# Kernel tuning notes

Hardware: AMD Instinct MI355X
Metric: run time of the kernel (lower is better)

Reference implementation:

```python
import jax, jax.numpy as jnp
import numpy as np

# Static multi-level feature-map shapes (H, W) per level.
SPATIAL_SHAPES = np.array([[92, 160], [46, 80], [23, 40], [12, 20]], dtype=np.int32)
NUM_HEADS = 8
NUM_LEVELS = 4
NUM_POINTS = 4      # sampling points per head per level (num_all_points)
NUM_Z = 4           # num_Z_anchors; NUM_POINTS % NUM_Z == 0
EMBED = 256
HEAD_DIM = EMBED // NUM_HEADS


def setup_inputs() -> dict:
    key = jax.random.key(0)
    ks = jax.random.split(key, 10)
    bs, nq = 2, 10000
    nv = int((SPATIAL_SHAPES[:, 0] * SPATIAL_SHAPES[:, 1]).sum())  # 19560
    query = jax.random.normal(ks[0], (bs, nq, EMBED), jnp.float32)
    value = jax.random.normal(ks[1], (bs, nv, EMBED), jnp.float32)
    query_pos = jax.random.normal(ks[2], (bs, nq, EMBED), jnp.float32)
    reference_points = jax.random.uniform(ks[3], (bs, nq, NUM_Z, 2), jnp.float32)
    W_val = jax.random.normal(ks[4], (EMBED, EMBED), jnp.float32) / jnp.sqrt(EMBED)
    b_val = jnp.zeros((EMBED,), jnp.float32)
    W_off = jax.random.normal(ks[5], (EMBED, NUM_HEADS * NUM_LEVELS * NUM_POINTS * 2), jnp.float32) * 0.01
    b_off = jax.random.normal(ks[6], (NUM_HEADS * NUM_LEVELS * NUM_POINTS * 2,), jnp.float32) * 0.5
    W_attn = jax.random.normal(ks[7], (EMBED, NUM_HEADS * NUM_LEVELS * NUM_POINTS), jnp.float32) * 0.02
    b_attn = jnp.zeros((NUM_HEADS * NUM_LEVELS * NUM_POINTS,), jnp.float32)
    spatial_shapes = jnp.asarray(SPATIAL_SHAPES)
    return {
        'query': query, 'value': value, 'query_pos': query_pos,
        'reference_points': reference_points,
        'W_val': W_val, 'b_val': b_val, 'W_off': W_off, 'b_off': b_off,
        'W_attn': W_attn, 'b_attn': b_attn, 'spatial_shapes': spatial_shapes,
    }


def _bilinear(v, x, y, H, W):
    """grid_sample(mode='bilinear', padding_mode='zeros', align_corners=False).

    v: (bs, H, W, heads, d); x, y: (bs, nq, heads, P) pixel coords.
    Returns (bs, nq, heads, P, d).
    """
    x0 = jnp.floor(x)
    y0 = jnp.floor(y)
    wx1 = x - x0
    wy1 = y - y0
    wx0 = 1.0 - wx1
    wy0 = 1.0 - wy1
    x0i = x0.astype(jnp.int32)
    y0i = y0.astype(jnp.int32)
    b = jnp.arange(v.shape[0])[:, None, None, None]
    h = jnp.arange(v.shape[3])[None, None, :, None]

    def gather(yi, xi):
        valid = (yi >= 0) & (yi < H) & (xi >= 0) & (xi < W)
        yc = jnp.clip(yi, 0, H - 1)
        xc = jnp.clip(xi, 0, W - 1)
        g = v[b, yc, xc, h]  # (bs, nq, heads, P, d)
        return g * valid[..., None].astype(v.dtype)

    return (gather(y0i, x0i) * (wy0 * wx0)[..., None]
            + gather(y0i, x0i + 1) * (wy0 * wx1)[..., None]
            + gather(y0i + 1, x0i) * (wy1 * wx0)[..., None]
            + gather(y0i + 1, x0i + 1) * (wy1 * wx1)[..., None])


def reference(query, value, query_pos, reference_points, W_val, b_val,
              W_off, b_off, W_attn, b_attn, spatial_shapes):
    bs, nq, _ = query.shape
    q = query + query_pos
    # value projection -> per-head values
    v = (value @ W_val + b_val).reshape(bs, -1, NUM_HEADS, HEAD_DIM)
    # sampling offsets and attention weights from query
    off = (q @ W_off + b_off).reshape(bs, nq, NUM_HEADS, NUM_LEVELS, NUM_POINTS, 2)
    attn = (q @ W_attn + b_attn).reshape(bs, nq, NUM_HEADS, NUM_LEVELS * NUM_POINTS)
    attn = jax.nn.softmax(attn, axis=-1).reshape(bs, nq, NUM_HEADS, NUM_LEVELS, NUM_POINTS)
    # normalize offsets by (w, h) of each level
    norm = jnp.stack([spatial_shapes[:, 1], spatial_shapes[:, 0]], -1).astype(q.dtype)  # (L, 2)
    off = off / norm[None, None, None, :, None, :]
    # fold Z-anchor reference points in, matching the shape[-1]==2 branch
    off = off.reshape(bs, nq, NUM_HEADS, NUM_LEVELS, NUM_POINTS // NUM_Z, NUM_Z, 2)
    loc = reference_points[:, :, None, None, None, :, :] + off
    loc = loc.reshape(bs, nq, NUM_HEADS, NUM_LEVELS, NUM_POINTS, 2)
    grid = 2.0 * loc - 1.0  # grid_sample convention

    start = 0
    sampled = []
    for lvl in range(NUM_LEVELS):
        H, W = int(SPATIAL_SHAPES[lvl, 0]), int(SPATIAL_SHAPES[lvl, 1])
        vl = v[:, start:start + H * W].reshape(bs, H, W, NUM_HEADS, HEAD_DIM)
        start += H * W
        # align_corners=False pixel coords
        x = ((grid[:, :, :, lvl, :, 0] + 1.0) * W - 1.0) * 0.5
        y = ((grid[:, :, :, lvl, :, 1] + 1.0) * H - 1.0) * 0.5
        sampled.append(_bilinear(vl, x, y, H, W))
    samp = jnp.stack(sampled, axis=3)  # (bs, nq, heads, L, P, d)
    out = (samp * attn[..., None]).sum(axis=(3, 4))  # (bs, nq, heads, d)
    return out.reshape(bs, nq, NUM_HEADS * HEAD_DIM)
```

## Files before the change

kernel.cpp:

```cpp
#include <hip/hip_runtime.h>

#define NQ 10000
#define BS 2
#define NV 19560
#define NH 8
#define HD 32
#define EMB 256

typedef __attribute__((ext_vector_type(8))) short bf16x8;
typedef __attribute__((ext_vector_type(4))) float f32x4;
typedef __attribute__((ext_vector_type(4))) short s16x4;

__device__ __forceinline__ unsigned short f2bf(float x) {
    unsigned u = __float_as_uint(x);
    u += 0x7FFFu + ((u >> 16) & 1u);
    return (unsigned short)(u >> 16);
}

__global__ __launch_bounds__(256) void convert_W(
    const float* __restrict__ Wv, const float* __restrict__ Wo,
    const float* __restrict__ Wa, const float* __restrict__ bv,
    const float* __restrict__ bo, const float* __restrict__ ba,
    ushort* __restrict__ Bt, float* __restrict__ bias) {
    int n = blockIdx.x;
    int k = threadIdx.x;
    float x;
    if (n < 256)       x = Wv[k * 256 + n];
    else if (n < 512)  x = Wo[k * 256 + (n - 256)];
    else               x = Wa[k * 128 + (n - 512)];
    Bt[n * 256 + k] = f2bf(x);
    if (k == 0)
        bias[n] = (n < 256) ? bv[n] : (n < 512) ? bo[n - 256] : ba[n - 512];
}

__global__ __launch_bounds__(256) void gemm_fused(
    const float* __restrict__ value, const float* __restrict__ query,
    const float* __restrict__ qpos, const ushort* __restrict__ Bt,
    const float* __restrict__ bias,
    ushort* __restrict__ Cv, float* __restrict__ C0, float* __restrict__ C1)
{
    __shared__ short As[64][40], Bhs[128][40];

    const int tid = threadIdx.x;
    const int bid = blockIdx.x;
    bool isval; int mblk, npan;
    if (bid < 1224) { isval = true;  mblk = bid >> 1; npan = bid & 1; }
    else { int q = bid - 1224; isval = false; mblk = q / 3; npan = q % 3; }

    const int M  = isval ? (BS * NV) : (BS * NQ);
    const int m0 = mblk * 64;
    const int n0 = npan * 128;
    const int nbase = (isval ? 0 : 256) + n0;

    const float* A = isval ? value : query;

    const int arow = tid >> 2;
    const int acol = (tid & 3) * 8;
    const bool aval = (m0 + arow) < M;
    const float* Ap  = A    + (size_t)(m0 + arow) * 256 + acol;
    const float* A2p = qpos + (size_t)(m0 + arow) * 256 + acol;
    const int brow = tid >> 1;
    const int bcol = (tid & 1) * 16;
    const ushort* Bp = Bt + (size_t)(nbase + brow) * 256 + bcol;

    const int lane = tid & 63, wave = tid >> 6;
    const int wrow = (wave >> 1) * 32, wcol = (wave & 1) * 64;
    const int lr = lane & 15, quad = lane >> 4, lk = quad * 8;

    f32x4 acc[2][4] = {};

    for (int k0 = 0; k0 < 256; k0 += 32) {
        #pragma unroll
        for (int g = 0; g < 2; g++) {
            f32x4 v = {};
            if (aval) {
                v = *(const f32x4*)(Ap + k0 + g * 4);
                if (!isval) v += *(const f32x4*)(A2p + k0 + g * 4);
            }
            s16x4 hh;
            #pragma unroll
            for (int e = 0; e < 4; e++) hh[e] = (short)f2bf(v[e]);
            *(s16x4*)&As[arow][acol + g * 4] = hh;
        }
        *(bf16x8*)&Bhs[brow][bcol]     = *(const bf16x8*)(Bp + k0);
        *(bf16x8*)&Bhs[brow][bcol + 8] = *(const bf16x8*)(Bp + k0 + 8);
        __syncthreads();

        bf16x8 af[2], bhf[4];
        #pragma unroll
        for (int i = 0; i < 2; i++)
            af[i] = *(const bf16x8*)&As[wrow + i * 16 + lr][lk];
        #pragma unroll
        for (int j = 0; j < 4; j++)
            bhf[j] = *(const bf16x8*)&Bhs[wcol + j * 16 + lr][lk];
        #pragma unroll
        for (int i = 0; i < 2; i++)
            #pragma unroll
            for (int j = 0; j < 4; j++)
                acc[i][j] = __builtin_amdgcn_mfma_f32_16x16x32_bf16(af[i], bhf[j], acc[i][j], 0, 0, 0);
        __syncthreads();
    }

    #pragma unroll
    for (int j = 0; j < 4; j++) {
        int cc = wcol + j * 16 + lr;
        int col = n0 + cc;
        float bb = bias[nbase + cc];
        #pragma unroll
        for (int i = 0; i < 2; i++) {
            int gmb = m0 + wrow + i * 16 + quad * 4;
            #pragma unroll
            for (int r = 0; r < 4; r++) {
                int gm = gmb + r;
                if (gm < M) {
                    float val = acc[i][j][r] + bb;
                    if (isval) {
                        int h = col >> 5, d = col & 31;
                        int b = (gm >= NV) ? 1 : 0;
                        int pix = gm - b * NV;
                        Cv[((size_t)(b * 8 + h) * NV + pix) * 32 + d] = f2bf(val);
                    } else {
                        if (col < 256) C0[(size_t)gm * 256 + col] = val;
                        else           C1[(size_t)gm * 128 + (col - 256)] = val;
                    }
                }
            }
        }
    }
}

__global__ __launch_bounds__(256) void sample4(
    const ushort* __restrict__ v, const float* __restrict__ off,
    const float* __restrict__ attn, const float* __restrict__ refp,
    float* __restrict__ out)
{
    __shared__ int   s_off[256][5];
    __shared__ float s_w[256][5];

    const int bq0 = blockIdx.x * 2;
    const int t = threadIdx.x;

    {
        const int bq = bq0 + (t >> 7);
        const int b = (bq >= NQ) ? 1 : 0;
        const int i = t & 127;
        const int h = i >> 4, l = (i >> 2) & 3, p = i & 3;

        float logit = attn[(size_t)bq * 128 + i];
        float mx = logit;
        #pragma unroll
        for (int m = 1; m < 16; m <<= 1) mx = fmaxf(mx, __shfl_xor(mx, m, 16));
        float e = __expf(logit - mx);
        float s = e;
        #pragma unroll
        for (int m = 1; m < 16; m <<= 1) s += __shfl_xor(s, m, 16);
        float w = e / s;

        const float Wf[4] = {160.f, 80.f, 40.f, 20.f};
        const float Hf[4] = {92.f, 46.f, 23.f, 12.f};
        const int   Wi[4] = {160, 80, 40, 20};
        const int   Hi[4] = {92, 46, 23, 12};
        const int   st[4] = {0, 14720, 18400, 19320};

        float ox = off[(size_t)bq * 256 + h * 32 + l * 8 + p * 2];
        float oy = off[(size_t)bq * 256 + h * 32 + l * 8 + p * 2 + 1];
        float rx = refp[(size_t)bq * 8 + p * 2];
        float ry = refp[(size_t)bq * 8 + p * 2 + 1];
        float x = rx * Wf[l] + ox - 0.5f;
        float y = ry * Hf[l] + oy - 0.5f;
        float x0f = floorf(x), y0f = floorf(y);
        float wx1 = x - x0f, wy1 = y - y0f;
        float wx0 = 1.f - wx1, wy0 = 1.f - wy1;
        int x0 = (int)x0f, y0 = (int)y0f;
        const int W = Wi[l], H = Hi[l];
        float mx0 = ((unsigned)x0       < (unsigned)W) ? 1.f : 0.f;
        float mx1 = ((unsigned)(x0 + 1) < (unsigned)W) ? 1.f : 0.f;
        float my0 = ((unsigned)y0       < (unsigned)H) ? 1.f : 0.f;
        float my1 = ((unsigned)(y0 + 1) < (unsigned)H) ? 1.f : 0.f;
        int xc0 = min(max(x0, 0), W - 1);
        int xc1 = min(max(x0 + 1, 0), W - 1);
        int yc0 = min(max(y0, 0), H - 1);
        int yc1 = min(max(y0 + 1, 0), H - 1);
        int base = ((b * 8 + h) * NV + st[l]) * 32;
        s_off[t][0] = base + (yc0 * W + xc0) * 32;
        s_off[t][1] = base + (yc0 * W + xc1) * 32;
        s_off[t][2] = base + (yc1 * W + xc0) * 32;
        s_off[t][3] = base + (yc1 * W + xc1) * 32;
        s_w[t][0] = w * wy0 * wx0 * my0 * mx0;
        s_w[t][1] = w * wy0 * wx1 * my0 * mx1;
        s_w[t][2] = w * wy1 * wx0 * my1 * mx0;
        s_w[t][3] = w * wy1 * wx1 * my1 * mx1;
    }
    __syncthreads();

    const int g = t >> 4;
    const int lane = t & 15;
    const int qi = g >> 3, h = g & 7;
    const int bq = bq0 + qi;
    const int d2 = lane * 2;
    const int pbase = qi * 128 + h * 16;

    float acc0 = 0.f, acc1 = 0.f, acc2 = 0.f, acc3 = 0.f;
    #pragma unroll
    for (int ib = 0; ib < 4; ib++) {
        int o[16]; float wgt[16];
        #pragma unroll
        for (int pp = 0; pp < 4; pp++) {
            int idx = pbase + ib * 4 + pp;
            #pragma unroll
            for (int c = 0; c < 4; c++) {
                o[pp * 4 + c]   = s_off[idx][c];
                wgt[pp * 4 + c] = s_w[idx][c];
            }
        }
        unsigned u[16];
        #pragma unroll
        for (int j = 0; j < 16; j++)
            u[j] = *(const unsigned*)(v + o[j] + d2);
        #pragma unroll
        for (int j = 0; j < 16; j += 2) {
            acc0 += wgt[j]     * __uint_as_float(u[j] << 16);
            acc1 += wgt[j]     * __uint_as_float(u[j] & 0xffff0000u);
            acc2 += wgt[j + 1] * __uint_as_float(u[j + 1] << 16);
            acc3 += wgt[j + 1] * __uint_as_float(u[j + 1] & 0xffff0000u);
        }
    }
    float2 res = make_float2(acc0 + acc2, acc1 + acc3);
    *(float2*)(out + (size_t)bq * 256 + h * 32 + d2) = res;
}

extern "C" void kernel_launch(void* const* d_in, const int* in_sizes, int n_in,
                              void* d_out, int out_size, void* d_ws, size_t ws_size,
                              hipStream_t stream) {
    const float* query     = (const float*)d_in[0];
    const float* value     = (const float*)d_in[1];
    const float* query_pos = (const float*)d_in[2];
    const float* refp      = (const float*)d_in[3];
    const float* W_val     = (const float*)d_in[4];
    const float* b_val     = (const float*)d_in[5];
    const float* W_off     = (const float*)d_in[6];
    const float* b_off     = (const float*)d_in[7];
    const float* W_attn    = (const float*)d_in[8];
    const float* b_attn    = (const float*)d_in[9];
    float* out = (float*)d_out;

    char* w = (char*)d_ws;
    float*  off    = (float*)w;   w += 20480000;
    float*  attn   = (float*)w;   w += 10240000;
    ushort* vp_bf  = (ushort*)w;  w += 20029440;
    ushort* Bt     = (ushort*)w;  w += 327680;
    float*  bias_c = (float*)w;   w += 2560;

    convert_W<<<640, 256, 0, stream>>>(W_val, W_off, W_attn, b_val, b_off, b_attn,
                                       Bt, bias_c);

    gemm_fused<<<1224 + 939, 256, 0, stream>>>(value, query, query_pos, Bt, bias_c,
                                               vp_bf, off, attn);

    sample4<<<BS * NQ / 2, 256, 0, stream>>>(vp_bf, off, attn, refp, out);
}
```

Measured before the change: 220.2 us.

## Load GEMM fragments directly from global memory, dropping LDS staging and barriers

The fused projection GEMM no longer stages A and B tiles through shared memory. Each wave loads its MFMA operand fragments straight from global memory and converts A to bf16 in registers, and the k-loop is fully unrolled. This removes LDS writes and reads and both __syncthreads per k-step. The cost is redundant global loads, since A rows are re-read by the two column waves and B rows by the two row waves, and the loads are narrower and less coalesced. Out-of-range rows are clamped to the last valid row rather than zeroed, and the epilogue still masks them.

```diff
diff --git a/kernel.cpp b/kernel.cpp
--- a/kernel.cpp
+++ b/kernel.cpp
@@ -39,8 +39,6 @@
     const float* __restrict__ bias,
     ushort* __restrict__ Cv, float* __restrict__ C0, float* __restrict__ C1)
 {
-    __shared__ short As[64][40], Bhs[128][40];
-
     const int tid = threadIdx.x;
     const int bid = blockIdx.x;
     bool isval; int mblk, npan;
@@ -54,51 +52,55 @@
 
     const float* A = isval ? value : query;
 
-    const int arow = tid >> 2;
-    const int acol = (tid & 3) * 8;
-    const bool aval = (m0 + arow) < M;
-    const float* Ap  = A    + (size_t)(m0 + arow) * 256 + acol;
-    const float* A2p = qpos + (size_t)(m0 + arow) * 256 + acol;
-    const int brow = tid >> 1;
-    const int bcol = (tid & 1) * 16;
-    const ushort* Bp = Bt + (size_t)(nbase + brow) * 256 + bcol;
-
     const int lane = tid & 63, wave = tid >> 6;
     const int wrow = (wave >> 1) * 32, wcol = (wave & 1) * 64;
     const int lr = lane & 15, quad = lane >> 4, lk = quad * 8;
 
+    const float* Ap[2]; const float* Qp[2];
+    #pragma unroll
+    for (int i = 0; i < 2; i++) {
+        int row = m0 + wrow + i * 16 + lr;
+        if (row >= M) row = M - 1;
+        Ap[i] = A    + (size_t)row * 256 + lk;
+        Qp[i] = qpos + (size_t)row * 256 + lk;
+    }
+    const ushort* Bp[4];
+    #pragma unroll
+    for (int j = 0; j < 4; j++)
+        Bp[j] = Bt + (size_t)(nbase + wcol + j * 16 + lr) * 256 + lk;
+
     f32x4 acc[2][4] = {};
 
+    #pragma unroll
     for (int k0 = 0; k0 < 256; k0 += 32) {
-        #pragma unroll
-        for (int g = 0; g < 2; g++) {
-            f32x4 v = {};
-            if (aval) {
-                v = *(const f32x4*)(Ap + k0 + g * 4);
-                if (!isval) v += *(const f32x4*)(A2p + k0 + g * 4);
-            }
-            s16x4 hh;
-            #pragma unroll
-            for (int e = 0; e < 4; e++) hh[e] = (short)f2bf(v[e]);
-            *(s16x4*)&As[arow][acol + g * 4] = hh;
-        }
-        *(bf16x8*)&Bhs[brow][bcol]     = *(const bf16x8*)(Bp + k0);
-        *(bf16x8*)&Bhs[brow][bcol + 8] = *(const bf16x8*)(Bp + k0 + 8);
-        __syncthreads();
-
-        bf16x8 af[2], bhf[4];
-        #pragma unroll
-        for (int i = 0; i < 2; i++)
-            af[i] = *(const bf16x8*)&As[wrow + i * 16 + lr][lk];
+        bf16x8 bhf[4];
         #pragma unroll
         for (int j = 0; j < 4; j++)
-            bhf[j] = *(const bf16x8*)&Bhs[wcol + j * 16 + lr][lk];
+            bhf[j] = *(const bf16x8*)(Bp[j] + k0);
+
+        bf16x8 af[2];
+        #pragma unroll
+        for (int i = 0; i < 2; i++) {
+            f32x4 lo = *(const f32x4*)(Ap[i] + k0);
+            f32x4 hi = *(const f32x4*)(Ap[i] + k0 + 4);
+            if (!isval) {
+                lo += *(const f32x4*)(Qp[i] + k0);
+                hi += *(const f32x4*)(Qp[i] + k0 + 4);
+            }
+            bf16x8 t;
+            #pragma unroll
+            for (int e = 0; e < 4; e++) {
+                t[e]     = (short)f2bf(lo[e]);
+                t[e + 4] = (short)f2bf(hi[e]);
+            }
+            af[i] = t;
+        }
+
         #pragma unroll
         for (int i = 0; i < 2; i++)
             #pragma unroll
             for (int j = 0; j < 4; j++)
                 acc[i][j] = __builtin_amdgcn_mfma_f32_16x16x32_bf16(af[i], bhf[j], acc[i][j], 0, 0, 0);
-        __syncthreads();
     }
 
     #pragma unroll
```

New measurement: 269.6 us. 22.4% more time.

## Double-buffer GEMM LDS tiles with register prefetch of next K slice

Applied to the files above, without the earlier changes.

The fused projection GEMM now keeps two LDS buffers for the A and B tiles. While MFMAs run on the current K slice, it loads the next slice from global memory into registers, then converts it to bf16 and stores it into the other buffer. This hides global-load latency behind compute and drops one of the two barriers per K step. In exchange it doubles the LDS footprint and raises register pressure, which could lower occupancy.

```diff
diff --git a/kernel.cpp b/kernel.cpp
--- a/kernel.cpp
+++ b/kernel.cpp
@@ -39,7 +39,8 @@
     const float* __restrict__ bias,
     ushort* __restrict__ Cv, float* __restrict__ C0, float* __restrict__ C1)
 {
-    __shared__ short As[64][40], Bhs[128][40];
+    __shared__ __align__(16) short As[2][64][40];
+    __shared__ __align__(16) short Bhs[2][128][40];
 
     const int tid = threadIdx.x;
     const int bid = blockIdx.x;
@@ -69,36 +70,73 @@
 
     f32x4 acc[2][4] = {};
 
-    for (int k0 = 0; k0 < 256; k0 += 32) {
+    {
         #pragma unroll
         for (int g = 0; g < 2; g++) {
             f32x4 v = {};
             if (aval) {
-                v = *(const f32x4*)(Ap + k0 + g * 4);
-                if (!isval) v += *(const f32x4*)(A2p + k0 + g * 4);
+                v = *(const f32x4*)(Ap + g * 4);
+                if (!isval) v += *(const f32x4*)(A2p + g * 4);
             }
             s16x4 hh;
             #pragma unroll
             for (int e = 0; e < 4; e++) hh[e] = (short)f2bf(v[e]);
-            *(s16x4*)&As[arow][acol + g * 4] = hh;
-        }
-        *(bf16x8*)&Bhs[brow][bcol]     = *(const bf16x8*)(Bp + k0);
-        *(bf16x8*)&Bhs[brow][bcol + 8] = *(const bf16x8*)(Bp + k0 + 8);
-        __syncthreads();
+            *(s16x4*)&As[0][arow][acol + g * 4] = hh;
+        }
+        *(bf16x8*)&Bhs[0][brow][bcol]     = *(const bf16x8*)(Bp);
+        *(bf16x8*)&Bhs[0][brow][bcol + 8] = *(const bf16x8*)(Bp + 8);
+    }
+    asm volatile("s_waitcnt lgkmcnt(0)" ::: "memory");
+    __builtin_amdgcn_s_barrier();
+
+    #pragma unroll
+    for (int s = 0; s < 8; s++) {
+        const int cur = s & 1, nxt = cur ^ 1;
+        const int k1 = (s + 1) * 32;
+
+        f32x4 pa0 = {}, pa1 = {}, qa0 = {}, qa1 = {};
+        bf16x8 pb0, pb1;
+        if (s < 7) {
+            if (aval) {
+                pa0 = *(const f32x4*)(Ap + k1);
+                pa1 = *(const f32x4*)(Ap + k1 + 4);
+                if (!isval) {
+                    qa0 = *(const f32x4*)(A2p + k1);
+                    qa1 = *(const f32x4*)(A2p + k1 + 4);
+                }
+            }
+            pb0 = *(const bf16x8*)(Bp + k1);
+            pb1 = *(const bf16x8*)(Bp + k1 + 8);
+        }
 
         bf16x8 af[2], bhf[4];
         #pragma unroll
         for (int i = 0; i < 2; i++)
-            af[i] = *(const bf16x8*)&As[wrow + i * 16 + lr][lk];
+            af[i] = *(const bf16x8*)&As[cur][wrow + i * 16 + lr][lk];
         #pragma unroll
         for (int j = 0; j < 4; j++)
-            bhf[j] = *(const bf16x8*)&Bhs[wcol + j * 16 + lr][lk];
+            bhf[j] = *(const bf16x8*)&Bhs[cur][wcol + j * 16 + lr][lk];
         #pragma unroll
         for (int i = 0; i < 2; i++)
             #pragma unroll
             for (int j = 0; j < 4; j++)
                 acc[i][j] = __builtin_amdgcn_mfma_f32_16x16x32_bf16(af[i], bhf[j], acc[i][j], 0, 0, 0);
-        __syncthreads();
+
+        if (s < 7) {
+            if (!isval) { pa0 += qa0; pa1 += qa1; }
+            bf16x8 t;
+            #pragma unroll
+            for (int e = 0; e < 4; e++) {
+                t[e]     = (short)f2bf(pa0[e]);
+                t[e + 4] = (short)f2bf(pa1[e]);
+            }
+            *(bf16x8*)&As[nxt][arow][acol & ~7] = t;
+            *(bf16x8*)&Bhs[nxt][brow][bcol]     = pb0;
+            *(bf16x8*)&Bhs[nxt][brow][bcol + 8] = pb1;
+
+            asm volatile("s_waitcnt lgkmcnt(0)" ::: "memory");
+            __builtin_amdgcn_s_barrier();
+        }
     }
 
     #pragma unroll
```

After: 221.9 us. No clear change (+0.8%).
